# Performance work log

Hardware: AMD Instinct MI355X
Metric: run time of the kernel (lower is better)

## Reference

```python
import jax, jax.numpy as jnp
import numpy as np

N = 50000
E = 800000
F_IN = 256
H = 64      # hidden_channels
NH = 4      # GAT heads

def setup_inputs() -> dict:
    key = jax.random.key(0)
    ks = jax.random.split(key, 16)
    x = jax.random.normal(ks[0], (N, F_IN), dtype=jnp.float32)
    edge_index = jax.random.randint(ks[1], (2, E), 0, N, dtype=jnp.int64)
    def w(k, shape, fan_in):
        return jax.random.normal(k, shape, dtype=jnp.float32) / np.sqrt(fan_in)
    return {
        "x": x, "edge_index": edge_index,
        "W1": w(ks[2], (F_IN, H), F_IN), "b1": jnp.zeros((H,), jnp.float32),
        "W2": w(ks[3], (H, H), H),       "b2": jnp.zeros((H,), jnp.float32),
        "Wg": w(ks[4], (H, NH * H), H),
        "att_src": w(ks[5], (NH, H), H), "att_dst": w(ks[6], (NH, H), H),
        "bg": jnp.zeros((NH * H,), jnp.float32),
        "Wf1": w(ks[7], (NH * H, H), NH * H), "bf1": jnp.zeros((H,), jnp.float32),
        "Wf2": w(ks[8], (H, 1), H),           "bf2": jnp.zeros((1,), jnp.float32),
    }

def _with_self_loops(edge_index):
    loops = jnp.arange(N, dtype=edge_index.dtype)
    src = jnp.concatenate([edge_index[0], loops])
    dst = jnp.concatenate([edge_index[1], loops])
    return src, dst

def _gcn(h, src, dst, W, b):
    # h: [N, d_in] -> [N, d_out]; symmetric norm D^-1/2 (A+I) D^-1/2
    h = h @ W
    deg = jax.ops.segment_sum(jnp.ones_like(dst, dtype=h.dtype), dst, num_segments=N)
    dinv = jnp.where(deg > 0, jax.lax.rsqrt(deg), 0.0)
    norm = dinv[src] * dinv[dst]                      # [E2]
    out = jax.ops.segment_sum(h[src] * norm[:, None], dst, num_segments=N)
    return out + b

def _gat(h, src, dst, Wg, att_src, att_dst, bg):
    hp = (h @ Wg).reshape(N, NH, H)                   # [N, NH, H]
    a_src = jnp.einsum('nhd,hd->nh', hp, att_src)     # [N, NH]
    a_dst = jnp.einsum('nhd,hd->nh', hp, att_dst)
    alpha = jax.nn.leaky_relu(a_src[src] + a_dst[dst], negative_slope=0.2)  # [E2, NH]
    amax = jax.ops.segment_max(alpha, dst, num_segments=N)
    e = jnp.exp(alpha - amax[dst])
    denom = jax.ops.segment_sum(e, dst, num_segments=N)
    coef = e / denom[dst]                             # [E2, NH]
    out = jax.ops.segment_sum(hp[src] * coef[:, :, None], dst, num_segments=N)
    return out.reshape(N, NH * H) + bg

def reference(x, edge_index, W1, b1, W2, b2, Wg, att_src, att_dst, bg, Wf1, bf1, Wf2, bf2):
    src, dst = _with_self_loops(edge_index)
    h = jax.nn.relu(_gcn(x, src, dst, W1, b1))        # dropout inactive (eval)
    h = jax.nn.relu(_gcn(h, src, dst, W2, b2))
    h = _gat(h, src, dst, Wg, att_src, att_dst, bg)
    h = jax.nn.relu(h @ Wf1 + bf1)
    return h @ Wf2 + bf2                              # [N, 1]
```

## Files before the change

### kernel.cpp

```cpp
#include <hip/hip_runtime.h>
#include <hip/hip_fp16.h>
#include <math.h>


#define CAP 64
#define CAPSH 6

typedef _Float16 v4h __attribute__((ext_vector_type(4)));
typedef float v4f __attribute__((ext_vector_type(4)));

__device__ __forceinline__ float lrelu02(float a) { return fmaxf(a, 0.2f * a); }

__device__ __forceinline__ float4 lrelu4(float4 a) {
    return make_float4(lrelu02(a.x), lrelu02(a.y), lrelu02(a.z), lrelu02(a.w));
}

__device__ __forceinline__ float4 exp4(float4 a) {
    return make_float4(__expf(a.x), __expf(a.y), __expf(a.z), __expf(a.w));
}

__device__ __forceinline__ float4 unpack4(float2 raw) {
    __half2 h01 = *(__half2*)&raw.x;
    __half2 h23 = *(__half2*)&raw.y;
    float2 f01 = __half22float2(h01);
    float2 f23 = __half22float2(h23);
    return make_float4(f01.x, f01.y, f23.x, f23.y);
}

__device__ __forceinline__ float2 pack4(float4 v) {
    float2 r;
    *(__half2*)&r.x = __float22half2_rn(make_float2(v.x, v.y));
    *(__half2*)&r.y = __float22half2_rn(make_float2(v.z, v.w));
    return r;
}


#define GEMM_BODY(BX, K, COLS)                                                     \
    __shared__ float As[16][68];                                                   \
    __shared__ float Bs[16][68];                                                   \
    const int row0 = (BX) * 64;                                                    \
    const int col0 = blockIdx.y * 64;                                              \
    const int t = threadIdx.x;                                                     \
    const int tx = t & 15;                                                         \
    const int ty = t >> 4;                                                         \
    const int lm = t >> 2;                                                         \
    const int lk4 = (t & 3) << 2;                                                  \
    const int wk = t >> 4;                                                         \
    const int wc = (t & 15) << 2;                                                  \
    float acc[4][4] = {};                                                          \
    for (int k0 = 0; k0 < K; k0 += 16) {                                           \
        float4 av = make_float4(0.f, 0.f, 0.f, 0.f);                               \
        int r = row0 + lm;                                                         \
        if (r < nrows) av = *(const float4*)(X + (size_t)r * K + k0 + lk4);        \
        As[lk4 + 0][lm] = av.x;                                                    \
        As[lk4 + 1][lm] = av.y;                                                    \
        As[lk4 + 2][lm] = av.z;                                                    \
        As[lk4 + 3][lm] = av.w;                                                    \
        *(float4*)&Bs[wk][wc] = *(const float4*)(W + (size_t)(k0 + wk) * COLS + col0 + wc); \
        __syncthreads();                                                           \
        _Pragma("unroll") for (int kk = 0; kk < 16; kk++) {                        \
            float4 a = *(const float4*)&As[kk][ty << 2];                           \
            float4 b = *(const float4*)&Bs[kk][tx << 2];                           \
            acc[0][0] = fmaf(a.x, b.x, acc[0][0]);                                 \
            acc[0][1] = fmaf(a.x, b.y, acc[0][1]);                                 \
            acc[0][2] = fmaf(a.x, b.z, acc[0][2]);                                 \
            acc[0][3] = fmaf(a.x, b.w, acc[0][3]);                                 \
            acc[1][0] = fmaf(a.y, b.x, acc[1][0]);                                 \
            acc[1][1] = fmaf(a.y, b.y, acc[1][1]);                                 \
            acc[1][2] = fmaf(a.y, b.z, acc[1][2]);                                 \
            acc[1][3] = fmaf(a.y, b.w, acc[1][3]);                                 \
            acc[2][0] = fmaf(a.z, b.x, acc[2][0]);                                 \
            acc[2][1] = fmaf(a.z, b.y, acc[2][1]);                                 \
            acc[2][2] = fmaf(a.z, b.z, acc[2][2]);                                 \
            acc[2][3] = fmaf(a.z, b.w, acc[2][3]);                                 \
            acc[3][0] = fmaf(a.w, b.x, acc[3][0]);                                 \
            acc[3][1] = fmaf(a.w, b.y, acc[3][1]);                                 \
            acc[3][2] = fmaf(a.w, b.z, acc[3][2]);                                 \
            acc[3][3] = fmaf(a.w, b.w, acc[3][3]);                                 \
        }                                                                          \
        __syncthreads();                                                           \
    }

__launch_bounds__(256)
__global__ void k_fused1(const int* __restrict__ src, const int* __restrict__ dst, int E,
                         int* __restrict__ cnt, unsigned short* __restrict__ slots,
                         const float* __restrict__ X, const float* __restrict__ W,
                         __half* __restrict__ Y, int nrows, int gemmBlocks,
                         const float* __restrict__ Wg, const float* __restrict__ att_src,
                         const float* __restrict__ att_dst, const float* __restrict__ Wf1,
                         const float* __restrict__ bf1, const float* __restrict__ bg,
                         const float* __restrict__ W2, float* __restrict__ watt,
                         __half* __restrict__ WcF, __half* __restrict__ W2F,
                         float* __restrict__ bias2) {
    if ((int)blockIdx.x >= gemmBlocks) {
        int b2 = blockIdx.x - gemmBlocks;
        int tt = threadIdx.x;
        if (b2 < 64) {
            int idx = b2 * 256 + tt;
            int r = idx >> 6, c = idx & 63;
            int h = r >> 6, k = r & 63;
            float s = 0.f;
            for (int j = 0; j < 64; j++)
                s = fmaf(Wg[k * 256 + h * 64 + j], Wf1[(h * 64 + j) * 64 + c], s);
            int ks = r >> 4, kr = r & 15;
            int lfrag = ((kr >> 2) << 4) | (c & 15);
            int jf = kr & 3;
            int w = c >> 4;
            WcF[((((w << 4) | ks) << 6) | lfrag) * 4 + jf] = __float2half_rn(s);
        } else if (b2 == 64) {
            for (int idx = tt; idx < 512; idx += 256) {
                int k = idx >> 3, c8 = idx & 7;
                int h = c8 & 3;
                const float* att = (c8 < 4) ? att_src : att_dst;
                float s = 0.f;
                for (int c = 0; c < 64; c++)
                    s = fmaf(Wg[k * 256 + h * 64 + c], att[h * 64 + c], s);
                watt[k * 8 + c8] = s;
            }
            if (tt < 64) {
                float s = bf1[tt];
                for (int j = 0; j < 256; j++) s = fmaf(bg[j], Wf1[j * 64 + tt], s);
                bias2[tt] = s;
            }
            for (int f = tt; f < 4096; f += 256) {
                int jf = f & 3, lfrag = (f >> 2) & 63, ws = f >> 8;
                int w = ws >> 2, ks = ws & 3;
                int k = ks * 16 + ((lfrag >> 4) << 2) + jf;
                int c = w * 16 + (lfrag & 15);
                W2F[f] = __float2half_rn(W2[k * 64 + c]);
            }
        } else {
            int e = (b2 - 65) * 256 + tt;
            if (e < E) {
                int d = dst[e];
                int p = atomicAdd(&cnt[d], 1);
                if (p < CAP) slots[((size_t)d << CAPSH) + p] = (unsigned short)src[e];
            }
        }
        return;
    }
    GEMM_BODY(blockIdx.x, 256, 64)
#pragma unroll
    for (int i = 0; i < 4; i++) {
        int row = row0 + (ty << 2) + i;
        if (row >= nrows) break;
        float4 o = make_float4(acc[i][0], acc[i][1], acc[i][2], acc[i][3]);
        ((float2*)(Y + (size_t)row * 64))[tx] = pack4(o);
    }
}


__launch_bounds__(256)
__global__ void k_prescale(__half* __restrict__ A, const int* __restrict__ cnt, int n) {
    int t = threadIdx.x;
    int l = t & 15;
    int v = blockIdx.x * 16 + (t >> 4);
    if (v >= n) return;
    float dv = rsqrtf((float)(cnt[v] + 1));
    float2 raw = ((const float2*)(A + (size_t)v * 64))[l];
    float4 f = unpack4(raw);
    f.x *= dv; f.y *= dv; f.z *= dv; f.w *= dv;
    ((float2*)(A + (size_t)v * 64))[l] = pack4(f);
}


__launch_bounds__(256)
__global__ void k_gcn1_gemm2(const __half* __restrict__ A, const unsigned short* __restrict__ slots,
                             const int* __restrict__ cnt, const float* __restrict__ b1,
                             const __half* __restrict__ W2F, __half* __restrict__ A2, int n) {
    __shared__ alignas(16) __half s_oh[16 * 68];
    __shared__ alignas(16) __half s_res[16 * 68];
    __shared__ float s_dv[16];
    int t = threadIdx.x;
    int lane = t & 63;
    int l = t & 15;
    int nb = t >> 4;
    int v = blockIdx.x * 16 + nb;
    bool act = (v < n);
    if (act) {
        int deg = min(cnt[v], CAP);
        const unsigned short* lst = slots + ((size_t)v << CAPSH);
        float dv = rsqrtf((float)(deg + 1));
        float4 a0 = unpack4(((const float2*)(A + (size_t)v * 64))[l]);
        float4 a1 = make_float4(0.f, 0.f, 0.f, 0.f);
        float4 a2 = a1, a3 = a1;
        int j = 0;
        for (; j + 7 < deg; j += 8) {
            ushort4 sa = *(const ushort4*)(lst + j);
            ushort4 sb = *(const ushort4*)(lst + j + 4);
            float4 t0 = unpack4(((const float2*)(A + (size_t)sa.x * 64))[l]);
            float4 t1 = unpack4(((const float2*)(A + (size_t)sa.y * 64))[l]);
            float4 t2 = unpack4(((const float2*)(A + (size_t)sa.z * 64))[l]);
            float4 t3 = unpack4(((const float2*)(A + (size_t)sa.w * 64))[l]);
            float4 t4 = unpack4(((const float2*)(A + (size_t)sb.x * 64))[l]);
            float4 t5 = unpack4(((const float2*)(A + (size_t)sb.y * 64))[l]);
            float4 t6 = unpack4(((const float2*)(A + (size_t)sb.z * 64))[l]);
            float4 t7 = unpack4(((const float2*)(A + (size_t)sb.w * 64))[l]);
            a0.x += t0.x + t4.x; a0.y += t0.y + t4.y; a0.z += t0.z + t4.z; a0.w += t0.w + t4.w;
            a1.x += t1.x + t5.x; a1.y += t1.y + t5.y; a1.z += t1.z + t5.z; a1.w += t1.w + t5.w;
            a2.x += t2.x + t6.x; a2.y += t2.y + t6.y; a2.z += t2.z + t6.z; a2.w += t2.w + t6.w;
            a3.x += t3.x + t7.x; a3.y += t3.y + t7.y; a3.z += t3.z + t7.z; a3.w += t3.w + t7.w;
        }
        for (; j + 3 < deg; j += 4) {
            ushort4 sa = *(const ushort4*)(lst + j);
            float4 t0 = unpack4(((const float2*)(A + (size_t)sa.x * 64))[l]);
            float4 t1 = unpack4(((const float2*)(A + (size_t)sa.y * 64))[l]);
            float4 t2 = unpack4(((const float2*)(A + (size_t)sa.z * 64))[l]);
            float4 t3 = unpack4(((const float2*)(A + (size_t)sa.w * 64))[l]);
            a0.x += t0.x; a0.y += t0.y; a0.z += t0.z; a0.w += t0.w;
            a1.x += t1.x; a1.y += t1.y; a1.z += t1.z; a1.w += t1.w;
            a2.x += t2.x; a2.y += t2.y; a2.z += t2.z; a2.w += t2.w;
            a3.x += t3.x; a3.y += t3.y; a3.z += t3.z; a3.w += t3.w;
        }
        for (; j < deg; j++) {
            float4 ta = unpack4(((const float2*)(A + (size_t)lst[j] * 64))[l]);
            a0.x += ta.x; a0.y += ta.y; a0.z += ta.z; a0.w += ta.w;
        }
        a0.x += a1.x + a2.x + a3.x;
        a0.y += a1.y + a2.y + a3.y;
        a0.z += a1.z + a2.z + a3.z;
        a0.w += a1.w + a2.w + a3.w;
        float4 b = ((const float4*)b1)[l];
        float4 o;
        o.x = fmaxf(fmaf(dv, a0.x, b.x), 0.f);
        o.y = fmaxf(fmaf(dv, a0.y, b.y), 0.f);
        o.z = fmaxf(fmaf(dv, a0.z, b.z), 0.f);
        o.w = fmaxf(fmaf(dv, a0.w, b.w), 0.f);
        *(float2*)&s_oh[nb * 68 + (l << 2)] = pack4(o);
        if (l == 0) s_dv[nb] = dv;
    } else {
        *(float2*)&s_oh[nb * 68 + (l << 2)] = make_float2(0.f, 0.f);
        if (l == 0) s_dv[nb] = 0.f;
    }
    __syncthreads();
    int w = t >> 6;
    v4f acc = {0.f, 0.f, 0.f, 0.f};
    int arow = (lane & 15) * 68;
    int acol = (lane >> 4) << 2;
#pragma unroll
    for (int ks = 0; ks < 4; ks++) {
        v4h a = *(const v4h*)&s_oh[arow + ks * 16 + acol];
        v4h bfr = *(const v4h*)&W2F[((((w << 2) | ks) << 6) | lane) << 2];
        acc = __builtin_amdgcn_mfma_f32_16x16x16f16(a, bfr, acc, 0, 0, 0);
    }
    int cc = (w << 4) | (lane & 15);
    int m0 = (lane >> 4) << 2;
#pragma unroll
    for (int j = 0; j < 4; j++)
        s_res[(m0 + j) * 68 + cc] = __float2half_rn(acc[j] * s_dv[m0 + j]);
    __syncthreads();
    if (act)
        ((float2*)(A2 + (size_t)v * 64))[l] = *(const float2*)&s_res[nb * 68 + (l << 2)];
}


__launch_bounds__(256)
__global__ void k_gcn2_att(const __half* __restrict__ T, const unsigned short* __restrict__ slots,
                           const int* __restrict__ cnt, const float* __restrict__ bias,
                           const float* __restrict__ watt, __half* __restrict__ Out,
                           float* __restrict__ asrc, float* __restrict__ adst, int n) {
    int t = threadIdx.x;
    int l = t & 15;
    int v = blockIdx.x * 16 + (t >> 4);
    if (v >= n) return;
    int deg = min(cnt[v], CAP);
    const unsigned short* lst = slots + ((size_t)v << CAPSH);
    float dv = rsqrtf((float)(deg + 1));
    float4 a0 = unpack4(((const float2*)(T + (size_t)v * 64))[l]);
    float4 a1 = make_float4(0.f, 0.f, 0.f, 0.f);
    float4 a2 = a1, a3 = a1;
    int j = 0;
    for (; j + 7 < deg; j += 8) {
        ushort4 sa = *(const ushort4*)(lst + j);
        ushort4 sb = *(const ushort4*)(lst + j + 4);
        float4 t0 = unpack4(((const float2*)(T + (size_t)sa.x * 64))[l]);
        float4 t1 = unpack4(((const float2*)(T + (size_t)sa.y * 64))[l]);
        float4 t2 = unpack4(((const float2*)(T + (size_t)sa.z * 64))[l]);
        float4 t3 = unpack4(((const float2*)(T + (size_t)sa.w * 64))[l]);
        float4 t4 = unpack4(((const float2*)(T + (size_t)sb.x * 64))[l]);
        float4 t5 = unpack4(((const float2*)(T + (size_t)sb.y * 64))[l]);
        float4 t6 = unpack4(((const float2*)(T + (size_t)sb.z * 64))[l]);
        float4 t7 = unpack4(((const float2*)(T + (size_t)sb.w * 64))[l]);
        a0.x += t0.x + t4.x; a0.y += t0.y + t4.y; a0.z += t0.z + t4.z; a0.w += t0.w + t4.w;
        a1.x += t1.x + t5.x; a1.y += t1.y + t5.y; a1.z += t1.z + t5.z; a1.w += t1.w + t5.w;
        a2.x += t2.x + t6.x; a2.y += t2.y + t6.y; a2.z += t2.z + t6.z; a2.w += t2.w + t6.w;
        a3.x += t3.x + t7.x; a3.y += t3.y + t7.y; a3.z += t3.z + t7.z; a3.w += t3.w + t7.w;
    }
    for (; j + 3 < deg; j += 4) {
        ushort4 sa = *(const ushort4*)(lst + j);
        float4 t0 = unpack4(((const float2*)(T + (size_t)sa.x * 64))[l]);
        float4 t1 = unpack4(((const float2*)(T + (size_t)sa.y * 64))[l]);
        float4 t2 = unpack4(((const float2*)(T + (size_t)sa.z * 64))[l]);
        float4 t3 = unpack4(((const float2*)(T + (size_t)sa.w * 64))[l]);
        a0.x += t0.x; a0.y += t0.y; a0.z += t0.z; a0.w += t0.w;
        a1.x += t1.x; a1.y += t1.y; a1.z += t1.z; a1.w += t1.w;
        a2.x += t2.x; a2.y += t2.y; a2.z += t2.z; a2.w += t2.w;
        a3.x += t3.x; a3.y += t3.y; a3.z += t3.z; a3.w += t3.w;
    }
    for (; j < deg; j++) {
        float4 ta = unpack4(((const float2*)(T + (size_t)lst[j] * 64))[l]);
        a0.x += ta.x; a0.y += ta.y; a0.z += ta.z; a0.w += ta.w;
    }
    a0.x += a1.x + a2.x + a3.x;
    a0.y += a1.y + a2.y + a3.y;
    a0.z += a1.z + a2.z + a3.z;
    a0.w += a1.w + a2.w + a3.w;
    float4 b = ((const float4*)bias)[l];
    float4 o;
    o.x = fmaxf(fmaf(dv, a0.x, b.x), 0.f);
    o.y = fmaxf(fmaf(dv, a0.y, b.y), 0.f);
    o.z = fmaxf(fmaf(dv, a0.z, b.z), 0.f);
    o.w = fmaxf(fmaf(dv, a0.w, b.w), 0.f);
    ((float2*)(Out + (size_t)v * 64))[l] = pack4(o);
    const float* wr = watt + (l << 2) * 8;
    float4 w0a = *(const float4*)(wr +  0), w0b = *(const float4*)(wr +  4);
    float4 w1a = *(const float4*)(wr +  8), w1b = *(const float4*)(wr + 12);
    float4 w2a = *(const float4*)(wr + 16), w2b = *(const float4*)(wr + 20);
    float4 w3a = *(const float4*)(wr + 24), w3b = *(const float4*)(wr + 28);
    float4 ds, dd;
    ds.x = o.x*w0a.x + o.y*w1a.x + o.z*w2a.x + o.w*w3a.x;
    ds.y = o.x*w0a.y + o.y*w1a.y + o.z*w2a.y + o.w*w3a.y;
    ds.z = o.x*w0a.z + o.y*w1a.z + o.z*w2a.z + o.w*w3a.z;
    ds.w = o.x*w0a.w + o.y*w1a.w + o.z*w2a.w + o.w*w3a.w;
    dd.x = o.x*w0b.x + o.y*w1b.x + o.z*w2b.x + o.w*w3b.x;
    dd.y = o.x*w0b.y + o.y*w1b.y + o.z*w2b.y + o.w*w3b.y;
    dd.z = o.x*w0b.z + o.y*w1b.z + o.z*w2b.z + o.w*w3b.z;
    dd.w = o.x*w0b.w + o.y*w1b.w + o.z*w2b.w + o.w*w3b.w;
    for (int off = 1; off <= 8; off <<= 1) {
        ds.x += __shfl_xor(ds.x, off); ds.y += __shfl_xor(ds.y, off);
        ds.z += __shfl_xor(ds.z, off); ds.w += __shfl_xor(ds.w, off);
        dd.x += __shfl_xor(dd.x, off); dd.y += __shfl_xor(dd.y, off);
        dd.z += __shfl_xor(dd.z, off); dd.w += __shfl_xor(dd.w, off);
    }
    if (l == 0) {
        ((float4*)asrc)[v] = ds;
        ((float4*)adst)[v] = dd;
    }
}


__launch_bounds__(256)
__global__ void k_gat_head(const __half* __restrict__ Bt, const unsigned short* __restrict__ slots,
                           const int* __restrict__ cnt, const float* __restrict__ asrc,
                           const float* __restrict__ adst, const __half* __restrict__ WcF,
                           const float* __restrict__ bias2, const float* __restrict__ Wf2,
                           const float* __restrict__ bf2, float* __restrict__ out, int n) {
    __shared__ alignas(16) __half s_aggh[16 * 260];
    __shared__ alignas(16) float s_e[16 * 68];
    __shared__ int s_sidx[16 * 17];
    __shared__ float s_part[16][4];
    int t = threadIdx.x;
    int lane = t & 63;
    int l = lane & 15;
    int nb = t >> 4;
    int v = blockIdx.x * 16 + nb;
    bool act = (v < n);
    if (act) {
        int deg = min(cnt[v], CAP);
        const unsigned short* lst = slots + ((size_t)v << CAPSH);
        float4 ad4 = ((const float4*)adst)[v];
        float4 as4 = ((const float4*)asrc)[v];
        float4 es = exp4(lrelu4(make_float4(as4.x + ad4.x, as4.y + ad4.y,
                                            as4.z + ad4.z, as4.w + ad4.w)));
        float4 esum = (l == 0) ? es : make_float4(0.f, 0.f, 0.f, 0.f);
        float4 bv = unpack4(((const float2*)(Bt + (size_t)v * 64))[l]);
        float4 acc0 = make_float4(es.x * bv.x, es.x * bv.y, es.x * bv.z, es.x * bv.w);
        float4 acc1 = make_float4(es.y * bv.x, es.y * bv.y, es.y * bv.z, es.y * bv.w);
        float4 acc2 = make_float4(es.z * bv.x, es.z * bv.y, es.z * bv.z, es.z * bv.w);
        float4 acc3 = make_float4(es.w * bv.x, es.w * bv.y, es.w * bv.z, es.w * bv.w);
        for (int c0 = 0; c0 < deg; c0 += 16) {
            int cl = min(16, deg - c0);
            float4 e = make_float4(0.f, 0.f, 0.f, 0.f);
            if (l < cl) {
                int s = lst[c0 + l];
                float4 sa = ((const float4*)asrc)[s];
                e = exp4(lrelu4(make_float4(sa.x + ad4.x, sa.y + ad4.y,
                                            sa.z + ad4.z, sa.w + ad4.w)));
                esum.x += e.x; esum.y += e.y; esum.z += e.z; esum.w += e.w;
                s_sidx[nb * 17 + l] = s;
            }
            *(float4*)&s_e[nb * 68 + (l << 2)] = e;
            __builtin_amdgcn_sched_barrier(0);
            for (int jj = 0; jj < cl; jj++) {
                int so = s_sidx[nb * 17 + jj];
                float4 ev = *(const float4*)&s_e[nb * 68 + (jj << 2)];
                float4 tv = unpack4(((const float2*)(Bt + (size_t)so * 64))[l]);
                acc0.x = fmaf(ev.x, tv.x, acc0.x); acc0.y = fmaf(ev.x, tv.y, acc0.y);
                acc0.z = fmaf(ev.x, tv.z, acc0.z); acc0.w = fmaf(ev.x, tv.w, acc0.w);
                acc1.x = fmaf(ev.y, tv.x, acc1.x); acc1.y = fmaf(ev.y, tv.y, acc1.y);
                acc1.z = fmaf(ev.y, tv.z, acc1.z); acc1.w = fmaf(ev.y, tv.w, acc1.w);
                acc2.x = fmaf(ev.z, tv.x, acc2.x); acc2.y = fmaf(ev.z, tv.y, acc2.y);
                acc2.z = fmaf(ev.z, tv.z, acc2.z); acc2.w = fmaf(ev.z, tv.w, acc2.w);
                acc3.x = fmaf(ev.w, tv.x, acc3.x); acc3.y = fmaf(ev.w, tv.y, acc3.y);
                acc3.z = fmaf(ev.w, tv.z, acc3.z); acc3.w = fmaf(ev.w, tv.w, acc3.w);
            }
        }
        for (int o = 8; o >= 1; o >>= 1) {
            esum.x += __shfl_xor(esum.x, o); esum.y += __shfl_xor(esum.y, o);
            esum.z += __shfl_xor(esum.z, o); esum.w += __shfl_xor(esum.w, o);
        }
        float i0 = 1.f / esum.x, i1 = 1.f / esum.y, i2 = 1.f / esum.z, i3 = 1.f / esum.w;
        *(float2*)&s_aggh[nb * 260 +   0 + (l << 2)] =
            pack4(make_float4(acc0.x*i0, acc0.y*i0, acc0.z*i0, acc0.w*i0));
        *(float2*)&s_aggh[nb * 260 +  64 + (l << 2)] =
            pack4(make_float4(acc1.x*i1, acc1.y*i1, acc1.z*i1, acc1.w*i1));
        *(float2*)&s_aggh[nb * 260 + 128 + (l << 2)] =
            pack4(make_float4(acc2.x*i2, acc2.y*i2, acc2.z*i2, acc2.w*i2));
        *(float2*)&s_aggh[nb * 260 + 192 + (l << 2)] =
            pack4(make_float4(acc3.x*i3, acc3.y*i3, acc3.z*i3, acc3.w*i3));
    } else {
        float2 z = make_float2(0.f, 0.f);
        *(float2*)&s_aggh[nb * 260 +   0 + (l << 2)] = z;
        *(float2*)&s_aggh[nb * 260 +  64 + (l << 2)] = z;
        *(float2*)&s_aggh[nb * 260 + 128 + (l << 2)] = z;
        *(float2*)&s_aggh[nb * 260 + 192 + (l << 2)] = z;
    }
    __syncthreads();
    int w = t >> 6;
    v4f accA = {0.f, 0.f, 0.f, 0.f};
    v4f accB = {0.f, 0.f, 0.f, 0.f};
    int arow = l * 260;
    int acol = (lane >> 4) << 2;
#pragma unroll
    for (int ks = 0; ks < 16; ks += 2) {
        v4h a0f = *(const v4h*)&s_aggh[arow + ks * 16 + acol];
        v4h b0f = *(const v4h*)&WcF[((((w << 4) | ks) << 6) | lane) << 2];
        accA = __builtin_amdgcn_mfma_f32_16x16x16f16(a0f, b0f, accA, 0, 0, 0);
        v4h a1f = *(const v4h*)&s_aggh[arow + (ks + 1) * 16 + acol];
        v4h b1f = *(const v4h*)&WcF[((((w << 4) | (ks + 1)) << 6) | lane) << 2];
        accB = __builtin_amdgcn_mfma_f32_16x16x16f16(a1f, b1f, accB, 0, 0, 0);
    }
    int cc = (w << 4) | l;
    float bb = bias2[cc], wq = Wf2[cc];
    float p0 = fmaxf(accA[0] + accB[0] + bb, 0.f) * wq;
    float p1 = fmaxf(accA[1] + accB[1] + bb, 0.f) * wq;
    float p2 = fmaxf(accA[2] + accB[2] + bb, 0.f) * wq;
    float p3 = fmaxf(accA[3] + accB[3] + bb, 0.f) * wq;
    for (int o = 1; o <= 8; o <<= 1) {
        p0 += __shfl_xor(p0, o); p1 += __shfl_xor(p1, o);
        p2 += __shfl_xor(p2, o); p3 += __shfl_xor(p3, o);
    }
    if (l == 0) {
        int m0 = (lane >> 4) << 2;
        s_part[m0 + 0][w] = p0; s_part[m0 + 1][w] = p1;
        s_part[m0 + 2][w] = p2; s_part[m0 + 3][w] = p3;
    }
    __syncthreads();
    if (t < 16 && blockIdx.x * 16 + t < n)
        out[blockIdx.x * 16 + t] =
            s_part[t][0] + s_part[t][1] + s_part[t][2] + s_part[t][3] + bf2[0];
}


extern "C" void kernel_launch(void* const* d_in, const int* in_sizes, int n_in,
                              void* d_out, int out_size, void* d_ws, size_t ws_size,
                              hipStream_t stream) {
    const float* x       = (const float*)d_in[0];
    const int*   ei      = (const int*)d_in[1];
    const float* W1      = (const float*)d_in[2];
    const float* b1      = (const float*)d_in[3];
    const float* W2      = (const float*)d_in[4];
    const float* b2      = (const float*)d_in[5];
    const float* Wg      = (const float*)d_in[6];
    const float* att_src = (const float*)d_in[7];
    const float* att_dst = (const float*)d_in[8];
    const float* bg      = (const float*)d_in[9];
    const float* Wf1     = (const float*)d_in[10];
    const float* bf1     = (const float*)d_in[11];
    const float* Wf2     = (const float*)d_in[12];
    const float* bf2     = (const float*)d_in[13];
    float* out = (float*)d_out;

    const int N = in_sizes[0] / 256;
    const int E = in_sizes[1] / 2;
    const int* src = ei;
    const int* dst = ei + E;

    char* p = (char*)d_ws;
    auto alloc = [&](size_t bytes) {
        void* r = (void*)p;
        p += (bytes + 255) & ~(size_t)255;
        return r;
    };
    __half* A   = (__half*)alloc((size_t)N * 64 * 2);
    __half* A2  = (__half*)alloc((size_t)N * 64 * 2);
    __half* B   = (__half*)alloc((size_t)N * 64 * 2);
    float* asrc = (float*)alloc((size_t)N * 4 * 4);
    float* adst = (float*)alloc((size_t)N * 4 * 4);
    int*   cnt  = (int*)alloc((size_t)N * 4);
    unsigned short* slots = (unsigned short*)alloc((size_t)N * CAP * 2);
    float* watt   = (float*)alloc(64 * 8 * 4);
    __half* WcF   = (__half*)alloc(256 * 64 * 2);
    __half* W2F   = (__half*)alloc(64 * 64 * 2);
    float* bias2  = (float*)alloc(64 * 4);

    const int gE = (E + 255) / 256;
    const int grow = (N + 63) / 64;
    const int gagg = (N + 15) / 16;

    hipMemsetAsync(cnt, 0, (size_t)N * 4, stream);

    k_fused1<<<grow + 65 + gE, 256, 0, stream>>>(
        src, dst, E, cnt, slots, x, W1, A, N, grow,
        Wg, att_src, att_dst, Wf1, bf1, bg, W2, watt, WcF, W2F, bias2);

    k_prescale<<<gagg, 256, 0, stream>>>(A, cnt, N);

    k_gcn1_gemm2<<<gagg, 256, 0, stream>>>(A, slots, cnt, b1, W2F, A2, N);

    k_gcn2_att<<<gagg, 256, 0, stream>>>(A2, slots, cnt, b2, watt, B, asrc, adst, N);

    k_gat_head<<<gagg, 256, 0, stream>>>(B, slots, cnt, asrc, adst,
                                         WcF, bias2, Wf2, bf2, out, N);
}
```

Baseline: 237.5 us.

## Fold degree prescale into GEMM epilogue and split edge scatter into own kernel

Edge bucketing moves out of the fused GEMM launch into a dedicated scatter kernel that runs first and handles four edges per thread, batching loads and atomics. Because degree counts are then ready before the first GEMM, that GEMM multiplies each output row by its rsqrt degree factor in the epilogue. This lets the separate prescale kernel go, removing a full read-modify-write pass over the fp16 feature matrix and one launch. The trade-off is that the scatter no longer overlaps with the GEMM blocks, and the degree now uses a count clamped to CAP, which can differ for nodes with more than CAP in-edges.

```diff
diff --git a/kernel.cpp b/kernel.cpp
--- a/kernel.cpp
+++ b/kernel.cpp
@@ -32,6 +32,31 @@
     *(__half2*)&r.x = __float22half2_rn(make_float2(v.x, v.y));
     *(__half2*)&r.y = __float22half2_rn(make_float2(v.z, v.w));
     return r;
+}
+
+
+__launch_bounds__(256)
+__global__ void k_scatter(const int* __restrict__ src, const int* __restrict__ dst, int E,
+                          int* __restrict__ cnt, unsigned short* __restrict__ slots) {
+    int tt = threadIdx.x;
+    int base = blockIdx.x * 1024 + tt;
+    int e0 = base, e1 = base + 256, e2 = base + 512, e3 = base + 768;
+    int d0 = (e0 < E) ? dst[e0] : 0;
+    int d1 = (e1 < E) ? dst[e1] : 0;
+    int d2 = (e2 < E) ? dst[e2] : 0;
+    int d3 = (e3 < E) ? dst[e3] : 0;
+    int s0 = (e0 < E) ? src[e0] : 0;
+    int s1 = (e1 < E) ? src[e1] : 0;
+    int s2 = (e2 < E) ? src[e2] : 0;
+    int s3 = (e3 < E) ? src[e3] : 0;
+    int p0 = (e0 < E) ? atomicAdd(&cnt[d0], 1) : CAP;
+    int p1 = (e1 < E) ? atomicAdd(&cnt[d1], 1) : CAP;
+    int p2 = (e2 < E) ? atomicAdd(&cnt[d2], 1) : CAP;
+    int p3 = (e3 < E) ? atomicAdd(&cnt[d3], 1) : CAP;
+    if (p0 < CAP) slots[((size_t)d0 << CAPSH) + p0] = (unsigned short)s0;
+    if (p1 < CAP) slots[((size_t)d1 << CAPSH) + p1] = (unsigned short)s1;
+    if (p2 < CAP) slots[((size_t)d2 << CAPSH) + p2] = (unsigned short)s2;
+    if (p3 < CAP) slots[((size_t)d3 << CAPSH) + p3] = (unsigned short)s3;
 }
 
 
@@ -82,8 +107,7 @@
     }
 
 __launch_bounds__(256)
-__global__ void k_fused1(const int* __restrict__ src, const int* __restrict__ dst, int E,
-                         int* __restrict__ cnt, unsigned short* __restrict__ slots,
+__global__ void k_fused1(const int* __restrict__ cnt,
                          const float* __restrict__ X, const float* __restrict__ W,
                          __half* __restrict__ Y, int nrows, int gemmBlocks,
                          const float* __restrict__ Wg, const float* __restrict__ att_src,
@@ -107,7 +131,7 @@
             int jf = kr & 3;
             int w = c >> 4;
             WcF[((((w << 4) | ks) << 6) | lfrag) * 4 + jf] = __float2half_rn(s);
-        } else if (b2 == 64) {
+        } else {
             for (int idx = tt; idx < 512; idx += 256) {
                 int k = idx >> 3, c8 = idx & 7;
                 int h = c8 & 3;
@@ -129,13 +153,6 @@
                 int c = w * 16 + (lfrag & 15);
                 W2F[f] = __float2half_rn(W2[k * 64 + c]);
             }
-        } else {
-            int e = (b2 - 65) * 256 + tt;
-            if (e < E) {
-                int d = dst[e];
-                int p = atomicAdd(&cnt[d], 1);
-                if (p < CAP) slots[((size_t)d << CAPSH) + p] = (unsigned short)src[e];
-            }
         }
         return;
     }
@@ -144,23 +161,11 @@
     for (int i = 0; i < 4; i++) {
         int row = row0 + (ty << 2) + i;
         if (row >= nrows) break;
-        float4 o = make_float4(acc[i][0], acc[i][1], acc[i][2], acc[i][3]);
+        float dv = rsqrtf((float)(min(cnt[row], CAP) + 1));
+        float4 o = make_float4(acc[i][0] * dv, acc[i][1] * dv,
+                               acc[i][2] * dv, acc[i][3] * dv);
         ((float2*)(Y + (size_t)row * 64))[tx] = pack4(o);
     }
-}
-
-
-__launch_bounds__(256)
-__global__ void k_prescale(__half* __restrict__ A, const int* __restrict__ cnt, int n) {
-    int t = threadIdx.x;
-    int l = t & 15;
-    int v = blockIdx.x * 16 + (t >> 4);
-    if (v >= n) return;
-    float dv = rsqrtf((float)(cnt[v] + 1));
-    float2 raw = ((const float2*)(A + (size_t)v * 64))[l];
-    float4 f = unpack4(raw);
-    f.x *= dv; f.y *= dv; f.z *= dv; f.w *= dv;
-    ((float2*)(A + (size_t)v * 64))[l] = pack4(f);
 }
 
 
@@ -494,17 +499,17 @@
     __half* W2F   = (__half*)alloc(64 * 64 * 2);
     float* bias2  = (float*)alloc(64 * 4);
 
-    const int gE = (E + 255) / 256;
+    const int gScat = (E + 1023) / 1024;
     const int grow = (N + 63) / 64;
     const int gagg = (N + 15) / 16;
 
     hipMemsetAsync(cnt, 0, (size_t)N * 4, stream);
 
-    k_fused1<<<grow + 65 + gE, 256, 0, stream>>>(
-        src, dst, E, cnt, slots, x, W1, A, N, grow,
+    k_scatter<<<gScat, 256, 0, stream>>>(src, dst, E, cnt, slots);
+
+    k_fused1<<<grow + 65, 256, 0, stream>>>(
+        cnt, x, W1, A, N, grow,
         Wg, att_src, att_dst, Wf1, bf1, bg, W2, watt, WcF, W2F, bias2);
-
-    k_prescale<<<gagg, 256, 0, stream>>>(A, cnt, N);
 
     k_gcn1_gemm2<<<gagg, 256, 0, stream>>>(A, slots, cnt, b1, W2F, A2, N);
 
```

Measured after the change: 264.1 us. +11.2%, slower.
